# Optimization experiments

Measured on AMD Instinct MI355X. Metric: run time of the kernel, lower is better.

Reference implementation:

```python
import jax, jax.numpy as jnp
import numpy as np

N_CLASSES = 300
EMPTY = N_CLASSES
ALPHA, GAMMA = 0.25, 2.0
W_CLS, W_DOA, W_LOUD, W_CONF, W_SCE = 1.0, 1.0, 0.5, 1.0, 0.3
L_CLS, L_DOA, L_CONF = 1.0, 1.0, 0.5  # matching cost weights


def _lsa(cost):
    """Rectangular linear sum assignment (Jonker-Volgenant / e-maxx Hungarian).
    Returns (row_idx, col_idx) matching min(P,G) pairs, same optimum as scipy."""
    transposed = cost.shape[0] > cost.shape[1]
    C = cost.T if transposed else cost
    n, m = C.shape  # n <= m
    INF = float('inf')
    u = [0.0] * (n + 1)
    v = [0.0] * (m + 1)
    p = [0] * (m + 1)
    for i in range(1, n + 1):
        p[0] = i
        j0 = 0
        minv = [INF] * (m + 1)
        way = [0] * (m + 1)
        used = [False] * (m + 1)
        while True:
            used[j0] = True
            i0 = p[j0]
            delta = INF
            j1 = 0
            for j in range(1, m + 1):
                if not used[j]:
                    cur = C[i0 - 1, j - 1] - u[i0] - v[j]
                    if cur < minv[j]:
                        minv[j] = cur
                        way[j] = j0
                    if minv[j] < delta:
                        delta = minv[j]
                        j1 = j
            for j in range(m + 1):
                if used[j]:
                    u[p[j]] += delta
                    v[j] -= delta
                else:
                    minv[j] -= delta
            j0 = j1
            if p[j0] == 0:
                break
        while j0:
            j1 = way[j0]
            p[j0] = p[j1]
            j0 = j1
    rows, cols = [], []
    for j in range(1, m + 1):
        if p[j]:
            rows.append(p[j] - 1)
            cols.append(j - 1)
    r = np.asarray(rows, np.int64)
    c = np.asarray(cols, np.int64)
    if transposed:
        r, c = c, r
    return r, c


def _match(cl, dv, conf, gcls, gdoa, gmask):
    """Per-frame Hungarian matching (no-grad, host numpy), faithful to hungarian_match.
    Returns matched mask (B,T,S) bool, per-slot target class (B,T,S) int32 (EMPTY if unmatched),
    and gather index into gt slots (B,T,S) int32 (0 where unmatched; masked out later)."""
    B, T, S, C = cl.shape
    z = cl - cl.max(-1, keepdims=True)
    prob = np.exp(z)
    prob /= prob.sum(-1, keepdims=True)
    prob = prob[..., :N_CLASSES]
    dn = dv / np.maximum(np.linalg.norm(dv, axis=-1, keepdims=True), 1e-12)
    cp = 1.0 / (1.0 + np.exp(-conf))
    matched = np.zeros((B, T, S), bool)
    tgt = np.full((B, T, S), EMPTY, np.int32)
    gidx = np.zeros((B, T, S), np.int32)
    for b in range(B):
        for t in range(T):
            act = np.nonzero(gmask[b, t])[0]
            if act.size == 0:
                continue
            gc = gcls[b, t, act]
            gd = gdoa[b, t, act]
            gdn = gd / np.maximum(np.linalg.norm(gd, axis=-1, keepdims=True), 1e-12)
            cost = (L_CLS * (-prob[b, t][:, gc])
                    + L_DOA * (1.0 - dn[b, t] @ gdn.T)
                    + L_CONF * (1.0 - cp[b, t])[:, None])
            r, c = _lsa(cost.astype(np.float64))
            matched[b, t, r] = True
            tgt[b, t, r] = gc[c]
            gidx[b, t, r] = act[c]
    return matched, tgt, gidx


def _loss(class_logits, doa_vec, loudness, confidence, sce_vec, gt_doa, gt_loud,
          matched, tgt_cls, gidx):
    B, T, S, _ = class_logits.shape
    dt = class_logits.dtype
    mf = matched.astype(dt)                      # (B,T,S)
    # focal loss (target = matched gt class, else EMPTY)
    logp = jax.nn.log_softmax(class_logits, axis=-1)
    ce = -jnp.take_along_axis(logp, tgt_cls[..., None].astype(jnp.int32), axis=-1)[..., 0]
    f = ALPHA * (1.0 - jnp.exp(-ce)) ** GAMMA * ce
    Gm = mf.sum(-1)                              # (B,T) matched count
    Um = S - Gm
    safeG = jnp.maximum(Gm, 1.0)
    safeU = jnp.maximum(Um, 1.0)
    cls_fr = (jnp.where(Gm > 0, (f * mf).sum(-1) / safeG, 0.0)
              + jnp.where(Um > 0, (f * (1.0 - mf)).sum(-1) / safeU, 0.0))
    # gather matched gt doa / loud per slot
    g3 = jnp.broadcast_to(gidx[..., None].astype(jnp.int32), gt_doa.shape)
    mdoa = jnp.take_along_axis(gt_doa, g3, axis=2)       # (B,T,S,3)
    mloud = jnp.take_along_axis(gt_loud, gidx.astype(jnp.int32), axis=2)
    # DOA cosine distance (torch cosine_similarity eps=1e-8)
    eps = 1e-8
    num = (doa_vec * mdoa).sum(-1)
    den = (jnp.maximum(jnp.linalg.norm(doa_vec, axis=-1), eps)
           * jnp.maximum(jnp.linalg.norm(mdoa, axis=-1), eps))
    d = 1.0 - num / den
    doa_fr = jnp.where(Gm > 0, (d * mf).sum(-1) / safeG, 0.0)
    # smooth L1 (beta=1)
    diff = loudness - mloud
    ad = jnp.abs(diff)
    sl1 = jnp.where(ad < 1.0, 0.5 * diff * diff, ad - 0.5)
    loud_fr = jnp.where(Gm > 0, (sl1 * mf).sum(-1) / safeG, 0.0)
    # BCE-with-logits, target = matched indicator (zeros if no gt)
    bce = jax.nn.softplus(confidence) - confidence * mf
    conf_fr = bce.mean(-1)
    # SCE: mse(sce, gt_doa * exp(gt_loud/20)) over matched slots
    gt_sce = mdoa * jnp.exp(mloud / 20.0)[..., None]
    sq = ((sce_vec - gt_sce) ** 2).mean(-1)
    sce_fr = jnp.where(Gm > 0, (sq * mf).sum(-1) / safeG, 0.0)
    norm = float(B * T)
    cls_l = W_CLS * cls_fr.sum() / norm
    doa_l = W_DOA * doa_fr.sum() / norm
    loud_l = W_LOUD * loud_fr.sum() / norm
    conf_l = W_CONF * conf_fr.sum() / norm
    sce_l = W_SCE * sce_fr.sum() / norm
    total = cls_l + doa_l + loud_l + conf_l + sce_l
    return jnp.stack([cls_l, doa_l, loud_l, conf_l, sce_l, total])


def setup_inputs() -> dict:
    key = jax.random.key(0)
    ks = jax.random.split(key, 9)
    B, T, S = 32, 256, 8
    C = N_CLASSES + 1
    return {
        "class_logits": jax.random.normal(ks[0], (B, T, S, C), jnp.float32),
        "doa_vec": jax.random.normal(ks[1], (B, T, S, 3), jnp.float32),
        "loudness": jax.random.normal(ks[2], (B, T, S), jnp.float32),
        "confidence": jax.random.normal(ks[3], (B, T, S), jnp.float32),
        "sce_vec": jax.random.normal(ks[4], (B, T, S, 3), jnp.float32),
        "gt_cls": jax.random.randint(ks[5], (B, T, S), 0, N_CLASSES, jnp.int32),
        "gt_doa": jax.random.normal(ks[6], (B, T, S, 3), jnp.float32),
        "gt_loud": jax.random.normal(ks[7], (B, T, S), jnp.float32),
        "gt_mask": jax.random.bernoulli(ks[8], 0.5, (B, T, S)),
    }


def reference(class_logits, doa_vec, loudness, confidence, sce_vec,
              gt_cls, gt_doa, gt_loud, gt_mask):
    matched, tgt, gidx = _match(np.asarray(class_logits), np.asarray(doa_vec),
                                np.asarray(confidence), np.asarray(gt_cls),
                                np.asarray(gt_doa), np.asarray(gt_mask))
    return _loss(class_logits, doa_vec, loudness, confidence, sce_vec,
                 gt_doa, gt_loud,
                 jnp.asarray(matched), jnp.asarray(tgt), jnp.asarray(gidx))
```

## Files before the change

kernel.cpp:

```cpp
#include <hip/hip_runtime.h>
#include <math.h>

#define NFRAMES 8192
#define NS 8
#define NC 301
#define NBLOCKS (NFRAMES / 4)

__device__ float g_partial[5 * NFRAMES];

__device__ __forceinline__ float readlanef(float x, int l) {
    return __int_as_float(__builtin_amdgcn_readlane(__float_as_int(x), l));
}

__global__ __launch_bounds__(256) void frame_kernel(
    const float* __restrict__ logits,
    const float* __restrict__ doa,
    const float* __restrict__ loud,
    const float* __restrict__ conf,
    const float* __restrict__ sce,
    const int*   __restrict__ gcls,
    const float* __restrict__ gdoa,
    const float* __restrict__ gloud,
    const unsigned int* __restrict__ gmaskw)
{
    __shared__ float lgs[4][NS * NC];

    const int lane = threadIdx.x & 63;
    const int wv   = threadIdx.x >> 6;
    const int f    = blockIdx.x * 4 + wv;
    const int s    = lane >> 3;
    const int g    = lane & 7;

    unsigned int mwd = gmaskw[lane];
    unsigned long long blo = __ballot((mwd & 0xFFFFFF00u) != 0);
    unsigned long long bf1 = __ballot(mwd == 0x3f800000u);
    const int mode = (blo == 0ull) ? 0 : (bf1 ? 2 : 1);

    {
        const float4* src = reinterpret_cast<const float4*>(logits + (size_t)f * (NS * NC));
        float4* dst = reinterpret_cast<float4*>(&lgs[wv][0]);
#pragma unroll
        for (int k = 0; k < 10; k++) {
            int idx = lane + (k << 6);
            if (idx < 602) dst[idx] = src[idx];
        }
    }

    float L_loud = 0.f, L_cf = 0.f, L_dx = 0.f, L_dy = 0.f, L_dz = 0.f;
    float L_s0 = 0.f, L_s1 = 0.f, L_s2 = 0.f;
    if (lane < 8) {
        size_t base = (size_t)f * NS + lane;
        L_loud = loud[base];  L_cf = conf[base];
        L_dx = doa[base * 3]; L_dy = doa[base * 3 + 1]; L_dz = doa[base * 3 + 2];
        L_s0 = sce[base * 3]; L_s1 = sce[base * 3 + 1]; L_s2 = sce[base * 3 + 2];
    }

    const float* ls = &lgs[wv][s * NC];

    float v[38];
#pragma unroll
    for (int k = 0; k < 38; k++) {
        int c = g + (k << 3);
        v[k] = (c < NC) ? ls[c] : -INFINITY;
    }
    float m0 = v[0], m1 = v[1], m2 = v[2], m3 = v[3];
#pragma unroll
    for (int k = 4; k + 3 < 38; k += 4) {
        m0 = fmaxf(m0, v[k]);     m1 = fmaxf(m1, v[k + 1]);
        m2 = fmaxf(m2, v[k + 2]); m3 = fmaxf(m3, v[k + 3]);
    }
    m0 = fmaxf(m0, v[36]); m1 = fmaxf(m1, v[37]);
    float m = fmaxf(fmaxf(m0, m1), fmaxf(m2, m3));
    m = fmaxf(m, __shfl_xor(m, 1, 8));
    m = fmaxf(m, __shfl_xor(m, 2, 8));
    m = fmaxf(m, __shfl_xor(m, 4, 8));
    float z0 = __expf(v[0] - m), z1 = __expf(v[1] - m);
    float z2 = __expf(v[2] - m), z3 = __expf(v[3] - m);
#pragma unroll
    for (int k = 4; k + 3 < 38; k += 4) {
        z0 += __expf(v[k] - m);     z1 += __expf(v[k + 1] - m);
        z2 += __expf(v[k + 2] - m); z3 += __expf(v[k + 3] - m);
    }
    z0 += __expf(v[36] - m); z1 += __expf(v[37] - m);
    float z = (z0 + z1) + (z2 + z3);
    z += __shfl_xor(z, 1, 8);
    z += __shfl_xor(z, 2, 8);
    z += __shfl_xor(z, 4, 8);
    const float A = m + __logf(z);
    const float lossA = __shfl(A, (lane & 7) << 3);

    int gcv = (lane < 8) ? gcls[f * NS + lane] : 0;
    int slotcls = __shfl(gcv, g);
    float myLgat = lgs[wv][s * NC + slotcls];
    float lossL300 = (lane < 8) ? lgs[wv][lane * NC + 300] : 0.f;

    bool on = false;
    if (lane < 8) {
        int idx = f * NS + lane;
        if (mode == 0)      on = ((const int*)gmaskw)[idx] != 0;
        else if (mode == 1) on = ((const unsigned char*)gmaskw)[idx] != 0;
        else                on = ((const float*)gmaskw)[idx] != 0.f;
    }
    unsigned long long bal = __ballot(on);
    const unsigned int actmask = (unsigned int)(bal & 0xFFull);
    const int G = __popc(actmask);

    int act_reg = 0;
    float gdx = 0.f, gdy = 0.f, gdz = 0.f;
    float rgx = 0.f, rgy = 0.f, rgz = 0.f, rgl = 0.f;
    if (lane < G) {
        unsigned int mk = actmask;
        for (int t = 0; t < lane; t++) mk &= mk - 1;
        int slot = __ffs(mk) - 1;
        act_reg = slot;
        size_t b3 = (size_t)(f * NS + slot) * 3;
        float x = gdoa[b3], y = gdoa[b3 + 1], zz = gdoa[b3 + 2];
        rgx = x; rgy = y; rgz = zz;
        rgl = gloud[(size_t)f * NS + slot];
        float n = fmaxf(sqrtf(x * x + y * y + zz * zz), 1e-12f);
        gdx = x / n; gdy = y / n; gdz = zz / n;
    }

    size_t sb3 = ((size_t)f * NS + s) * 3;
    float dxr = doa[sb3], dyr = doa[sb3 + 1], dzr = doa[sb3 + 2];
    float nn = fmaxf(sqrtf(dxr * dxr + dyr * dyr + dzr * dzr), 1e-12f);
    float dnx = dxr / nn, dny = dyr / nn, dnz = dzr / nn;
    float cp = 1.f / (1.f + __expf(-conf[(size_t)f * NS + s]));

    int   ag = __shfl(act_reg, g);
    float gx = __shfl(gdx, g), gy = __shfl(gdy, g), gz = __shfl(gdz, g);
    float lgt_c = __shfl(myLgat, (lane & 56) | ag);
    float costreg = INFINITY;
    if (g < G) {
        float pr = __expf(lgt_c - A);
        float dt = dnx * gx + dny * gy + dnz * gz;
        costreg = -pr + (1.f - dt) + 0.5f * (1.f - cp);
    }

    float d0 = (lane == 0) ? 0.f : INFINITY;
    float d1 = INFINITY, d2 = INFINITY, d3 = INFINITY;
    unsigned int par0 = 0, par1 = 0, par2 = 0, par3 = 0;

    for (int i = 0; i < G; i++) {
        float cc0 = readlanef(costreg,      i);
        float cc1 = readlanef(costreg,  8 + i);
        float cc2 = readlanef(costreg, 16 + i);
        float cc3 = readlanef(costreg, 24 + i);
        float cc4 = readlanef(costreg, 32 + i);
        float cc5 = readlanef(costreg, 40 + i);
        float cc6 = readlanef(costreg, 48 + i);
        float cc7 = readlanef(costreg, 56 + i);

        float n0, n1, n2, n3; int b0i, b1i, b2i, b3i;

#define DP_LOW6(dk, bestv, bestb)                                                    \
        {                                                                            \
            float best = INFINITY; int bb = 0; float nb, cand;                       \
            nb = __shfl_xor(dk, 1);  cand = (lane & 1)  ? nb + cc0 : INFINITY; if (cand < best) { best = cand; bb = 0; } \
            nb = __shfl_xor(dk, 2);  cand = (lane & 2)  ? nb + cc1 : INFINITY; if (cand < best) { best = cand; bb = 1; } \
            nb = __shfl_xor(dk, 4);  cand = (lane & 4)  ? nb + cc2 : INFINITY; if (cand < best) { best = cand; bb = 2; } \
            nb = __shfl_xor(dk, 8);  cand = (lane & 8)  ? nb + cc3 : INFINITY; if (cand < best) { best = cand; bb = 3; } \
            nb = __shfl_xor(dk, 16); cand = (lane & 16) ? nb + cc4 : INFINITY; if (cand < best) { best = cand; bb = 4; } \
            nb = __shfl_xor(dk, 32); cand = (lane & 32) ? nb + cc5 : INFINITY; if (cand < best) { best = cand; bb = 5; } \
            bestv = best; bestb = bb;                                                \
        }

        DP_LOW6(d0, n0, b0i)
        DP_LOW6(d1, n1, b1i)
        DP_LOW6(d2, n2, b2i)
        DP_LOW6(d3, n3, b3i)
#undef DP_LOW6
        { float cand = d0 + cc6; if (cand < n1) { n1 = cand; b1i = 6; } }
        { float cand = d2 + cc6; if (cand < n3) { n3 = cand; b3i = 6; } }
        { float cand = d0 + cc7; if (cand < n2) { n2 = cand; b2i = 7; } }
        { float cand = d1 + cc7; if (cand < n3) { n3 = cand; b3i = 7; } }

        d0 = n0; d1 = n1; d2 = n2; d3 = n3;
        int sh = 3 * i;
        par0 |= (unsigned)b0i << sh;
        par1 |= (unsigned)b1i << sh;
        par2 |= (unsigned)b2i << sh;
        par3 |= (unsigned)b3i << sh;
    }

    int mm_ = 0, mygt = 0;
    if (G > 0) {
        float vv = d0; int bm = lane;
        if (d1 < vv) { vv = d1; bm = lane | 64; }
        if (d2 < vv) { vv = d2; bm = lane | 128; }
        if (d3 < vv) { vv = d3; bm = lane | 192; }
        for (int o = 1; o < 64; o <<= 1) {
            float ov = __shfl_xor(vv, o);
            int   om = __shfl_xor(bm, o);
            if (ov < vv || (ov == vv && om < bm)) { vv = ov; bm = om; }
        }
        int mask = bm;
        for (int i = G - 1; i >= 0; i--) {
            int owner = mask & 63, kk = mask >> 6;
            unsigned qsel = (kk == 0) ? par0 : (kk == 1) ? par1
                          : (kk == 2) ? par2 : par3;
            unsigned qv = (unsigned)__builtin_amdgcn_readlane((int)qsel, owner);
            int p = (qv >> (3 * i)) & 7;
            if (lane == p) { mm_ = 1; mygt = i; }
            mask ^= 1 << p;
        }
    }

    int   gidx_v = __shfl(act_reg, mygt);
    float lgt_m  = __shfl(myLgat, ((lane & 7) << 3) + gidx_v);
    float mdx = __shfl(rgx, mygt), mdy = __shfl(rgy, mygt), mdz = __shfl(rgz, mygt);
    float ml  = __shfl(rgl, mygt);

    if (lane < 8) {
        int ss = lane;
        float mf = (float)mm_;
        float lgt = mm_ ? lgt_m : lossL300;
        float ce = lossA - lgt;
        float t1 = 1.f - __expf(-ce);
        float fce = 0.25f * t1 * t1 * ce;

        float num = L_dx * mdx + L_dy * mdy + L_dz * mdz;
        float den = fmaxf(sqrtf(L_dx * L_dx + L_dy * L_dy + L_dz * L_dz), 1e-8f) *
                    fmaxf(sqrtf(mdx * mdx + mdy * mdy + mdz * mdz), 1e-8f);
        float dterm = 1.f - num / den;

        float diff = L_loud - ml;
        float ad = fabsf(diff);
        float sl1 = (ad < 1.f) ? 0.5f * diff * diff : (ad - 0.5f);

        float sp = fmaxf(L_cf, 0.f) + __logf(1.f + __expf(-fabsf(L_cf)));
        float bce = sp - L_cf * mf;

        float el = __expf(ml * 0.05f);
        float e0 = L_s0 - mdx * el;
        float e1 = L_s1 - mdy * el;
        float e2 = L_s2 - mdz * el;
        float sq = (e0 * e0 + e1 * e1 + e2 * e2) * (1.f / 3.f);

        float c_m  = fce * mf;
        float c_u  = fce * (1.f - mf);
        float dsum = dterm * mf;
        float lsum = sl1 * mf;
        float qsum = sq * mf;
        float bsum = bce;
        for (int o = 1; o < 8; o <<= 1) {
            c_m  += __shfl_xor(c_m,  o, 8);
            c_u  += __shfl_xor(c_u,  o, 8);
            dsum += __shfl_xor(dsum, o, 8);
            lsum += __shfl_xor(lsum, o, 8);
            qsum += __shfl_xor(qsum, o, 8);
            bsum += __shfl_xor(bsum, o, 8);
        }
        if (ss == 0) {
            float Gm = (float)G, Um = (float)(NS - G);
            g_partial[0 * NFRAMES + f] = (G > 0 ? c_m / Gm : 0.f) + (G < NS ? c_u / Um : 0.f);
            g_partial[1 * NFRAMES + f] = (G > 0) ? dsum / Gm : 0.f;
            g_partial[2 * NFRAMES + f] = (G > 0) ? lsum / Gm : 0.f;
            g_partial[3 * NFRAMES + f] = bsum * (1.f / 8.f);
            g_partial[4 * NFRAMES + f] = (G > 0) ? qsum / Gm : 0.f;
        }
    }
}

__global__ __launch_bounds__(1024) void reduce_kernel(float* __restrict__ out) {
    __shared__ float red[16][5];
    const int tid  = threadIdx.x;
    const int lane = tid & 63;
    const int w    = tid >> 6;

    float a[5];
#pragma unroll
    for (int k = 0; k < 5; k++) {
        float lcl = 0.f;
        for (int i = tid; i < NFRAMES; i += 1024) lcl += g_partial[k * NFRAMES + i];
#pragma unroll
        for (int o = 1; o < 64; o <<= 1) lcl += __shfl_xor(lcl, o);
        a[k] = lcl;
    }
    if (lane == 0) {
#pragma unroll
        for (int k = 0; k < 5; k++) red[w][k] = a[k];
    }
    __syncthreads();
    if (tid == 0) {
        float acc[5] = {0.f, 0.f, 0.f, 0.f, 0.f};
        for (int ww = 0; ww < 16; ww++)
#pragma unroll
            for (int k = 0; k < 5; k++) acc[k] += red[ww][k];
        const float inv_norm = 1.f / (float)NFRAMES;
        float cls_l  = 1.0f * acc[0] * inv_norm;
        float doa_l  = 1.0f * acc[1] * inv_norm;
        float loud_l = 0.5f * acc[2] * inv_norm;
        float conf_l = 1.0f * acc[3] * inv_norm;
        float sce_l  = 0.3f * acc[4] * inv_norm;
        out[0] = cls_l; out[1] = doa_l; out[2] = loud_l;
        out[3] = conf_l; out[4] = sce_l;
        out[5] = cls_l + doa_l + loud_l + conf_l + sce_l;
    }
}

extern "C" void kernel_launch(void* const* d_in, const int* in_sizes, int n_in,
                              void* d_out, int out_size, void* d_ws, size_t ws_size,
                              hipStream_t stream) {
    const float* logits = (const float*)d_in[0];
    const float* doa    = (const float*)d_in[1];
    const float* loudn  = (const float*)d_in[2];
    const float* confi  = (const float*)d_in[3];
    const float* sce    = (const float*)d_in[4];
    const int*   gcls   = (const int*)d_in[5];
    const float* gdoa   = (const float*)d_in[6];
    const float* gloud  = (const float*)d_in[7];
    const unsigned int* gmask = (const unsigned int*)d_in[8];
    float* out = (float*)d_out;

    frame_kernel<<<NBLOCKS, 256, 0, stream>>>(logits, doa, loudn, confi, sce,
                                              gcls, gdoa, gloud, gmask);
    reduce_kernel<<<1, 1024, 0, stream>>>(out);
}
```

Before: 50.01 us.

## Pipeline per-wave frame loop with double-buffered direct global-to-LDS loads

Each block becomes a single wave that handles four frames in sequence. While the current frame is processed, the next frame's logits are prefetched into a second LDS buffer using global_load_lds, with explicit vmcnt waits. The goal is to hide global load latency behind the Hungarian DP and softmax work and to skip the register round-trip of the old copy. In exchange there are fewer waves per block, serial frames per wave, and hand-written waitcnt counts that must match the number of loads issued.

```diff
diff --git a/kernel.cpp b/kernel.cpp
--- a/kernel.cpp
+++ b/kernel.cpp
@@ -4,7 +4,11 @@
 #define NFRAMES 8192
 #define NS 8
 #define NC 301
-#define NBLOCKS (NFRAMES / 4)
+#define FPW 4
+#define NBLOCKS (NFRAMES / FPW)
+
+#define GLOBAL_AS __attribute__((address_space(1)))
+#define LDS_AS    __attribute__((address_space(3)))
 
 __device__ float g_partial[5 * NFRAMES];
 
@@ -12,7 +16,7 @@
     return __int_as_float(__builtin_amdgcn_readlane(__float_as_int(x), l));
 }
 
-__global__ __launch_bounds__(256) void frame_kernel(
+__global__ __launch_bounds__(64, 2) void frame_kernel(
     const float* __restrict__ logits,
     const float* __restrict__ doa,
     const float* __restrict__ loud,
@@ -23,243 +27,266 @@
     const float* __restrict__ gloud,
     const unsigned int* __restrict__ gmaskw)
 {
-    __shared__ float lgs[4][NS * NC];
-
-    const int lane = threadIdx.x & 63;
-    const int wv   = threadIdx.x >> 6;
-    const int f    = blockIdx.x * 4 + wv;
-    const int s    = lane >> 3;
-    const int g    = lane & 7;
+    __shared__ float lgs[2][NS * NC];
+
+    const int lane = threadIdx.x;
+    const int fbase = blockIdx.x * FPW;
+    const int s = lane >> 3;
+    const int g = lane & 7;
 
     unsigned int mwd = gmaskw[lane];
     unsigned long long blo = __ballot((mwd & 0xFFFFFF00u) != 0);
     unsigned long long bf1 = __ballot(mwd == 0x3f800000u);
     const int mode = (blo == 0ull) ? 0 : (bf1 ? 2 : 1);
 
-    {
-        const float4* src = reinterpret_cast<const float4*>(logits + (size_t)f * (NS * NC));
-        float4* dst = reinterpret_cast<float4*>(&lgs[wv][0]);
-#pragma unroll
-        for (int k = 0; k < 10; k++) {
-            int idx = lane + (k << 6);
-            if (idx < 602) dst[idx] = src[idx];
-        }
-    }
-
-    float L_loud = 0.f, L_cf = 0.f, L_dx = 0.f, L_dy = 0.f, L_dz = 0.f;
-    float L_s0 = 0.f, L_s1 = 0.f, L_s2 = 0.f;
-    if (lane < 8) {
-        size_t base = (size_t)f * NS + lane;
-        L_loud = loud[base];  L_cf = conf[base];
-        L_dx = doa[base * 3]; L_dy = doa[base * 3 + 1]; L_dz = doa[base * 3 + 2];
-        L_s0 = sce[base * 3]; L_s1 = sce[base * 3 + 1]; L_s2 = sce[base * 3 + 2];
-    }
-
-    const float* ls = &lgs[wv][s * NC];
-
-    float v[38];
-#pragma unroll
-    for (int k = 0; k < 38; k++) {
-        int c = g + (k << 3);
-        v[k] = (c < NC) ? ls[c] : -INFINITY;
-    }
-    float m0 = v[0], m1 = v[1], m2 = v[2], m3 = v[3];
-#pragma unroll
-    for (int k = 4; k + 3 < 38; k += 4) {
-        m0 = fmaxf(m0, v[k]);     m1 = fmaxf(m1, v[k + 1]);
-        m2 = fmaxf(m2, v[k + 2]); m3 = fmaxf(m3, v[k + 3]);
-    }
-    m0 = fmaxf(m0, v[36]); m1 = fmaxf(m1, v[37]);
-    float m = fmaxf(fmaxf(m0, m1), fmaxf(m2, m3));
-    m = fmaxf(m, __shfl_xor(m, 1, 8));
-    m = fmaxf(m, __shfl_xor(m, 2, 8));
-    m = fmaxf(m, __shfl_xor(m, 4, 8));
-    float z0 = __expf(v[0] - m), z1 = __expf(v[1] - m);
-    float z2 = __expf(v[2] - m), z3 = __expf(v[3] - m);
-#pragma unroll
-    for (int k = 4; k + 3 < 38; k += 4) {
-        z0 += __expf(v[k] - m);     z1 += __expf(v[k + 1] - m);
-        z2 += __expf(v[k + 2] - m); z3 += __expf(v[k + 3] - m);
-    }
-    z0 += __expf(v[36] - m); z1 += __expf(v[37] - m);
-    float z = (z0 + z1) + (z2 + z3);
-    z += __shfl_xor(z, 1, 8);
-    z += __shfl_xor(z, 2, 8);
-    z += __shfl_xor(z, 4, 8);
-    const float A = m + __logf(z);
-    const float lossA = __shfl(A, (lane & 7) << 3);
-
-    int gcv = (lane < 8) ? gcls[f * NS + lane] : 0;
-    int slotcls = __shfl(gcv, g);
-    float myLgat = lgs[wv][s * NC + slotcls];
-    float lossL300 = (lane < 8) ? lgs[wv][lane * NC + 300] : 0.f;
-
-    bool on = false;
-    if (lane < 8) {
-        int idx = f * NS + lane;
-        if (mode == 0)      on = ((const int*)gmaskw)[idx] != 0;
-        else if (mode == 1) on = ((const unsigned char*)gmaskw)[idx] != 0;
-        else                on = ((const float*)gmaskw)[idx] != 0.f;
-    }
-    unsigned long long bal = __ballot(on);
-    const unsigned int actmask = (unsigned int)(bal & 0xFFull);
-    const int G = __popc(actmask);
-
-    int act_reg = 0;
-    float gdx = 0.f, gdy = 0.f, gdz = 0.f;
-    float rgx = 0.f, rgy = 0.f, rgz = 0.f, rgl = 0.f;
-    if (lane < G) {
-        unsigned int mk = actmask;
-        for (int t = 0; t < lane; t++) mk &= mk - 1;
-        int slot = __ffs(mk) - 1;
-        act_reg = slot;
-        size_t b3 = (size_t)(f * NS + slot) * 3;
-        float x = gdoa[b3], y = gdoa[b3 + 1], zz = gdoa[b3 + 2];
-        rgx = x; rgy = y; rgz = zz;
-        rgl = gloud[(size_t)f * NS + slot];
-        float n = fmaxf(sqrtf(x * x + y * y + zz * zz), 1e-12f);
-        gdx = x / n; gdy = y / n; gdz = zz / n;
-    }
-
-    size_t sb3 = ((size_t)f * NS + s) * 3;
-    float dxr = doa[sb3], dyr = doa[sb3 + 1], dzr = doa[sb3 + 2];
-    float nn = fmaxf(sqrtf(dxr * dxr + dyr * dyr + dzr * dzr), 1e-12f);
-    float dnx = dxr / nn, dny = dyr / nn, dnz = dzr / nn;
-    float cp = 1.f / (1.f + __expf(-conf[(size_t)f * NS + s]));
-
-    int   ag = __shfl(act_reg, g);
-    float gx = __shfl(gdx, g), gy = __shfl(gdy, g), gz = __shfl(gdz, g);
-    float lgt_c = __shfl(myLgat, (lane & 56) | ag);
-    float costreg = INFINITY;
-    if (g < G) {
-        float pr = __expf(lgt_c - A);
-        float dt = dnx * gx + dny * gy + dnz * gz;
-        costreg = -pr + (1.f - dt) + 0.5f * (1.f - cp);
-    }
-
-    float d0 = (lane == 0) ? 0.f : INFINITY;
-    float d1 = INFINITY, d2 = INFINITY, d3 = INFINITY;
-    unsigned int par0 = 0, par1 = 0, par2 = 0, par3 = 0;
-
-    for (int i = 0; i < G; i++) {
-        float cc0 = readlanef(costreg,      i);
-        float cc1 = readlanef(costreg,  8 + i);
-        float cc2 = readlanef(costreg, 16 + i);
-        float cc3 = readlanef(costreg, 24 + i);
-        float cc4 = readlanef(costreg, 32 + i);
-        float cc5 = readlanef(costreg, 40 + i);
-        float cc6 = readlanef(costreg, 48 + i);
-        float cc7 = readlanef(costreg, 56 + i);
-
-        float n0, n1, n2, n3; int b0i, b1i, b2i, b3i;
+#define STAGE(FR, B)                                                            \
+    {                                                                           \
+        const float4* src_ = reinterpret_cast<const float4*>(                   \
+            logits + (size_t)(FR) * (NS * NC));                                 \
+        char* dstb_ = reinterpret_cast<char*>(&lgs[(B)][0]);                    \
+        _Pragma("unroll")                                                       \
+        for (int k = 0; k < 9; k++) {                                           \
+            __builtin_amdgcn_global_load_lds(                                   \
+                (const GLOBAL_AS void*)(src_ + (k << 6) + lane),                \
+                (LDS_AS void*)(dstb_ + (k << 10)), 16, 0, 0);                   \
+        }                                                                       \
+        if (lane < 602 - 576) {                                                 \
+            __builtin_amdgcn_global_load_lds(                                   \
+                (const GLOBAL_AS void*)(src_ + 576 + lane),                     \
+                (LDS_AS void*)(dstb_ + 9 * 1024), 16, 0, 0);                    \
+        }                                                                       \
+    }
+
+    STAGE(fbase, 0)
+
+#pragma unroll
+    for (int t = 0; t < FPW; t++) {
+        const int f = fbase + t;
+        const float* buf = &lgs[t & 1][0];
+
+        if (t + 1 < FPW) {
+            STAGE(f + 1, (t + 1) & 1)
+            asm volatile("s_waitcnt vmcnt(10)" ::: "memory");
+        } else {
+            asm volatile("s_waitcnt vmcnt(0)" ::: "memory");
+        }
+
+        float L_loud = 0.f, L_cf = 0.f, L_dx = 0.f, L_dy = 0.f, L_dz = 0.f;
+        float L_s0 = 0.f, L_s1 = 0.f, L_s2 = 0.f;
+        if (lane < 8) {
+            size_t base = (size_t)f * NS + lane;
+            L_loud = loud[base];  L_cf = conf[base];
+            L_dx = doa[base * 3]; L_dy = doa[base * 3 + 1]; L_dz = doa[base * 3 + 2];
+            L_s0 = sce[base * 3]; L_s1 = sce[base * 3 + 1]; L_s2 = sce[base * 3 + 2];
+        }
+        int gcv = (lane < 8) ? gcls[f * NS + lane] : 0;
+
+        size_t sb3 = ((size_t)f * NS + s) * 3;
+        float dxr = doa[sb3], dyr = doa[sb3 + 1], dzr = doa[sb3 + 2];
+        float nn = fmaxf(sqrtf(dxr * dxr + dyr * dyr + dzr * dzr), 1e-12f);
+        float dnx = dxr / nn, dny = dyr / nn, dnz = dzr / nn;
+        float cp = 1.f / (1.f + __expf(-conf[(size_t)f * NS + s]));
+
+        const float* ls = buf + s * NC;
+
+        float v[38];
+#pragma unroll
+        for (int k = 0; k < 38; k++) {
+            int c = g + (k << 3);
+            v[k] = (c < NC) ? ls[c] : -INFINITY;
+        }
+        float m0 = v[0], m1 = v[1], m2 = v[2], m3 = v[3];
+#pragma unroll
+        for (int k = 4; k + 3 < 38; k += 4) {
+            m0 = fmaxf(m0, v[k]);     m1 = fmaxf(m1, v[k + 1]);
+            m2 = fmaxf(m2, v[k + 2]); m3 = fmaxf(m3, v[k + 3]);
+        }
+        m0 = fmaxf(m0, v[36]); m1 = fmaxf(m1, v[37]);
+        float m = fmaxf(fmaxf(m0, m1), fmaxf(m2, m3));
+        m = fmaxf(m, __shfl_xor(m, 1, 8));
+        m = fmaxf(m, __shfl_xor(m, 2, 8));
+        m = fmaxf(m, __shfl_xor(m, 4, 8));
+        float z0 = __expf(v[0] - m), z1 = __expf(v[1] - m);
+        float z2 = __expf(v[2] - m), z3 = __expf(v[3] - m);
+#pragma unroll
+        for (int k = 4; k + 3 < 38; k += 4) {
+            z0 += __expf(v[k] - m);     z1 += __expf(v[k + 1] - m);
+            z2 += __expf(v[k + 2] - m); z3 += __expf(v[k + 3] - m);
+        }
+        z0 += __expf(v[36] - m); z1 += __expf(v[37] - m);
+        float z = (z0 + z1) + (z2 + z3);
+        z += __shfl_xor(z, 1, 8);
+        z += __shfl_xor(z, 2, 8);
+        z += __shfl_xor(z, 4, 8);
+        const float A = m + __logf(z);
+        const float lossA = __shfl(A, (lane & 7) << 3);
+
+        int slotcls = __shfl(gcv, g);
+        float myLgat = buf[s * NC + slotcls];
+        float lossL300 = (lane < 8) ? buf[lane * NC + 300] : 0.f;
+
+        bool on = false;
+        if (lane < 8) {
+            int idx = f * NS + lane;
+            if (mode == 0)      on = ((const int*)gmaskw)[idx] != 0;
+            else if (mode == 1) on = ((const unsigned char*)gmaskw)[idx] != 0;
+            else                on = ((const float*)gmaskw)[idx] != 0.f;
+        }
+        unsigned long long bal = __ballot(on);
+        const unsigned int actmask = (unsigned int)(bal & 0xFFull);
+        const int G = __popc(actmask);
+
+        int act_reg = 0;
+        float gdx = 0.f, gdy = 0.f, gdz = 0.f;
+        float rgx = 0.f, rgy = 0.f, rgz = 0.f, rgl = 0.f;
+        if (lane < G) {
+            unsigned int mk = actmask;
+            for (int tt = 0; tt < lane; tt++) mk &= mk - 1;
+            int slot = __ffs(mk) - 1;
+            act_reg = slot;
+            size_t b3 = (size_t)(f * NS + slot) * 3;
+            float x = gdoa[b3], y = gdoa[b3 + 1], zz = gdoa[b3 + 2];
+            rgx = x; rgy = y; rgz = zz;
+            rgl = gloud[(size_t)f * NS + slot];
+            float n = fmaxf(sqrtf(x * x + y * y + zz * zz), 1e-12f);
+            gdx = x / n; gdy = y / n; gdz = zz / n;
+        }
+
+        int   ag = __shfl(act_reg, g);
+        float gx = __shfl(gdx, g), gy = __shfl(gdy, g), gz = __shfl(gdz, g);
+        float lgt_c = __shfl(myLgat, (lane & 56) | ag);
+        float costreg = INFINITY;
+        if (g < G) {
+            float pr = __expf(lgt_c - A);
+            float dt = dnx * gx + dny * gy + dnz * gz;
+            costreg = -pr + (1.f - dt) + 0.5f * (1.f - cp);
+        }
+
+        float d0 = (lane == 0) ? 0.f : INFINITY;
+        float d1 = INFINITY, d2 = INFINITY, d3 = INFINITY;
+        unsigned int par0 = 0, par1 = 0, par2 = 0, par3 = 0;
+
+        for (int i = 0; i < G; i++) {
+            float cc0 = readlanef(costreg,      i);
+            float cc1 = readlanef(costreg,  8 + i);
+            float cc2 = readlanef(costreg, 16 + i);
+            float cc3 = readlanef(costreg, 24 + i);
+            float cc4 = readlanef(costreg, 32 + i);
+            float cc5 = readlanef(costreg, 40 + i);
+            float cc6 = readlanef(costreg, 48 + i);
+            float cc7 = readlanef(costreg, 56 + i);
+
+            float n0, n1, n2, n3; int b0i, b1i, b2i, b3i;
 
 #define DP_LOW6(dk, bestv, bestb)                                                    \
-        {                                                                            \
-            float best = INFINITY; int bb = 0; float nb, cand;                       \
-            nb = __shfl_xor(dk, 1);  cand = (lane & 1)  ? nb + cc0 : INFINITY; if (cand < best) { best = cand; bb = 0; } \
-            nb = __shfl_xor(dk, 2);  cand = (lane & 2)  ? nb + cc1 : INFINITY; if (cand < best) { best = cand; bb = 1; } \
-            nb = __shfl_xor(dk, 4);  cand = (lane & 4)  ? nb + cc2 : INFINITY; if (cand < best) { best = cand; bb = 2; } \
-            nb = __shfl_xor(dk, 8);  cand = (lane & 8)  ? nb + cc3 : INFINITY; if (cand < best) { best = cand; bb = 3; } \
-            nb = __shfl_xor(dk, 16); cand = (lane & 16) ? nb + cc4 : INFINITY; if (cand < best) { best = cand; bb = 4; } \
-            nb = __shfl_xor(dk, 32); cand = (lane & 32) ? nb + cc5 : INFINITY; if (cand < best) { best = cand; bb = 5; } \
-            bestv = best; bestb = bb;                                                \
-        }
-
-        DP_LOW6(d0, n0, b0i)
-        DP_LOW6(d1, n1, b1i)
-        DP_LOW6(d2, n2, b2i)
-        DP_LOW6(d3, n3, b3i)
+            {                                                                        \
+                float best = INFINITY; int bb = 0; float nb, cand;                   \
+                nb = __shfl_xor(dk, 1);  cand = (lane & 1)  ? nb + cc0 : INFINITY; if (cand < best) { best = cand; bb = 0; } \
+                nb = __shfl_xor(dk, 2);  cand = (lane & 2)  ? nb + cc1 : INFINITY; if (cand < best) { best = cand; bb = 1; } \
+                nb = __shfl_xor(dk, 4);  cand = (lane & 4)  ? nb + cc2 : INFINITY; if (cand < best) { best = cand; bb = 2; } \
+                nb = __shfl_xor(dk, 8);  cand = (lane & 8)  ? nb + cc3 : INFINITY; if (cand < best) { best = cand; bb = 3; } \
+                nb = __shfl_xor(dk, 16); cand = (lane & 16) ? nb + cc4 : INFINITY; if (cand < best) { best = cand; bb = 4; } \
+                nb = __shfl_xor(dk, 32); cand = (lane & 32) ? nb + cc5 : INFINITY; if (cand < best) { best = cand; bb = 5; } \
+                bestv = best; bestb = bb;                                            \
+            }
+
+            DP_LOW6(d0, n0, b0i)
+            DP_LOW6(d1, n1, b1i)
+            DP_LOW6(d2, n2, b2i)
+            DP_LOW6(d3, n3, b3i)
 #undef DP_LOW6
-        { float cand = d0 + cc6; if (cand < n1) { n1 = cand; b1i = 6; } }
-        { float cand = d2 + cc6; if (cand < n3) { n3 = cand; b3i = 6; } }
-        { float cand = d0 + cc7; if (cand < n2) { n2 = cand; b2i = 7; } }
-        { float cand = d1 + cc7; if (cand < n3) { n3 = cand; b3i = 7; } }
-
-        d0 = n0; d1 = n1; d2 = n2; d3 = n3;
-        int sh = 3 * i;
-        par0 |= (unsigned)b0i << sh;
-        par1 |= (unsigned)b1i << sh;
-        par2 |= (unsigned)b2i << sh;
-        par3 |= (unsigned)b3i << sh;
-    }
-
-    int mm_ = 0, mygt = 0;
-    if (G > 0) {
-        float vv = d0; int bm = lane;
-        if (d1 < vv) { vv = d1; bm = lane | 64; }
-        if (d2 < vv) { vv = d2; bm = lane | 128; }
-        if (d3 < vv) { vv = d3; bm = lane | 192; }
-        for (int o = 1; o < 64; o <<= 1) {
-            float ov = __shfl_xor(vv, o);
-            int   om = __shfl_xor(bm, o);
-            if (ov < vv || (ov == vv && om < bm)) { vv = ov; bm = om; }
-        }
-        int mask = bm;
-        for (int i = G - 1; i >= 0; i--) {
-            int owner = mask & 63, kk = mask >> 6;
-            unsigned qsel = (kk == 0) ? par0 : (kk == 1) ? par1
-                          : (kk == 2) ? par2 : par3;
-            unsigned qv = (unsigned)__builtin_amdgcn_readlane((int)qsel, owner);
-            int p = (qv >> (3 * i)) & 7;
-            if (lane == p) { mm_ = 1; mygt = i; }
-            mask ^= 1 << p;
-        }
-    }
-
-    int   gidx_v = __shfl(act_reg, mygt);
-    float lgt_m  = __shfl(myLgat, ((lane & 7) << 3) + gidx_v);
-    float mdx = __shfl(rgx, mygt), mdy = __shfl(rgy, mygt), mdz = __shfl(rgz, mygt);
-    float ml  = __shfl(rgl, mygt);
-
-    if (lane < 8) {
-        int ss = lane;
-        float mf = (float)mm_;
-        float lgt = mm_ ? lgt_m : lossL300;
-        float ce = lossA - lgt;
-        float t1 = 1.f - __expf(-ce);
-        float fce = 0.25f * t1 * t1 * ce;
-
-        float num = L_dx * mdx + L_dy * mdy + L_dz * mdz;
-        float den = fmaxf(sqrtf(L_dx * L_dx + L_dy * L_dy + L_dz * L_dz), 1e-8f) *
-                    fmaxf(sqrtf(mdx * mdx + mdy * mdy + mdz * mdz), 1e-8f);
-        float dterm = 1.f - num / den;
-
-        float diff = L_loud - ml;
-        float ad = fabsf(diff);
-        float sl1 = (ad < 1.f) ? 0.5f * diff * diff : (ad - 0.5f);
-
-        float sp = fmaxf(L_cf, 0.f) + __logf(1.f + __expf(-fabsf(L_cf)));
-        float bce = sp - L_cf * mf;
-
-        float el = __expf(ml * 0.05f);
-        float e0 = L_s0 - mdx * el;
-        float e1 = L_s1 - mdy * el;
-        float e2 = L_s2 - mdz * el;
-        float sq = (e0 * e0 + e1 * e1 + e2 * e2) * (1.f / 3.f);
-
-        float c_m  = fce * mf;
-        float c_u  = fce * (1.f - mf);
-        float dsum = dterm * mf;
-        float lsum = sl1 * mf;
-        float qsum = sq * mf;
-        float bsum = bce;
-        for (int o = 1; o < 8; o <<= 1) {
-            c_m  += __shfl_xor(c_m,  o, 8);
-            c_u  += __shfl_xor(c_u,  o, 8);
-            dsum += __shfl_xor(dsum, o, 8);
-            lsum += __shfl_xor(lsum, o, 8);
-            qsum += __shfl_xor(qsum, o, 8);
-            bsum += __shfl_xor(bsum, o, 8);
-        }
-        if (ss == 0) {
-            float Gm = (float)G, Um = (float)(NS - G);
-            g_partial[0 * NFRAMES + f] = (G > 0 ? c_m / Gm : 0.f) + (G < NS ? c_u / Um : 0.f);
-            g_partial[1 * NFRAMES + f] = (G > 0) ? dsum / Gm : 0.f;
-            g_partial[2 * NFRAMES + f] = (G > 0) ? lsum / Gm : 0.f;
-            g_partial[3 * NFRAMES + f] = bsum * (1.f / 8.f);
-            g_partial[4 * NFRAMES + f] = (G > 0) ? qsum / Gm : 0.f;
-        }
-    }
+            { float cand = d0 + cc6; if (cand < n1) { n1 = cand; b1i = 6; } }
+            { float cand = d2 + cc6; if (cand < n3) { n3 = cand; b3i = 6; } }
+            { float cand = d0 + cc7; if (cand < n2) { n2 = cand; b2i = 7; } }
+            { float cand = d1 + cc7; if (cand < n3) { n3 = cand; b3i = 7; } }
+
+            d0 = n0; d1 = n1; d2 = n2; d3 = n3;
+            int sh = 3 * i;
+            par0 |= (unsigned)b0i << sh;
+            par1 |= (unsigned)b1i << sh;
+            par2 |= (unsigned)b2i << sh;
+            par3 |= (unsigned)b3i << sh;
+        }
+
+        int mm_ = 0, mygt = 0;
+        if (G > 0) {
+            float vv = d0; int bm = lane;
+            if (d1 < vv) { vv = d1; bm = lane | 64; }
+            if (d2 < vv) { vv = d2; bm = lane | 128; }
+            if (d3 < vv) { vv = d3; bm = lane | 192; }
+            for (int o = 1; o < 64; o <<= 1) {
+                float ov = __shfl_xor(vv, o);
+                int   om = __shfl_xor(bm, o);
+                if (ov < vv || (ov == vv && om < bm)) { vv = ov; bm = om; }
+            }
+            int mask = bm;
+            for (int i = G - 1; i >= 0; i--) {
+                int owner = mask & 63, kk = mask >> 6;
+                unsigned qsel = (kk == 0) ? par0 : (kk == 1) ? par1
+                              : (kk == 2) ? par2 : par3;
+                unsigned qv = (unsigned)__builtin_amdgcn_readlane((int)qsel, owner);
+                int p = (qv >> (3 * i)) & 7;
+                if (lane == p) { mm_ = 1; mygt = i; }
+                mask ^= 1 << p;
+            }
+        }
+
+        int   gidx_v = __shfl(act_reg, mygt);
+        float lgt_m  = __shfl(myLgat, ((lane & 7) << 3) + gidx_v);
+        float mdx = __shfl(rgx, mygt), mdy = __shfl(rgy, mygt), mdz = __shfl(rgz, mygt);
+        float ml  = __shfl(rgl, mygt);
+
+        if (lane < 8) {
+            int ss = lane;
+            float mf = (float)mm_;
+            float lgt = mm_ ? lgt_m : lossL300;
+            float ce = lossA - lgt;
+            float t1 = 1.f - __expf(-ce);
+            float fce = 0.25f * t1 * t1 * ce;
+
+            float num = L_dx * mdx + L_dy * mdy + L_dz * mdz;
+            float den = fmaxf(sqrtf(L_dx * L_dx + L_dy * L_dy + L_dz * L_dz), 1e-8f) *
+                        fmaxf(sqrtf(mdx * mdx + mdy * mdy + mdz * mdz), 1e-8f);
+            float dterm = 1.f - num / den;
+
+            float diff = L_loud - ml;
+            float ad = fabsf(diff);
+            float sl1 = (ad < 1.f) ? 0.5f * diff * diff : (ad - 0.5f);
+
+            float sp = fmaxf(L_cf, 0.f) + __logf(1.f + __expf(-fabsf(L_cf)));
+            float bce = sp - L_cf * mf;
+
+            float el = __expf(ml * 0.05f);
+            float e0 = L_s0 - mdx * el;
+            float e1 = L_s1 - mdy * el;
+            float e2 = L_s2 - mdz * el;
+            float sq = (e0 * e0 + e1 * e1 + e2 * e2) * (1.f / 3.f);
+
+            float c_m  = fce * mf;
+            float c_u  = fce * (1.f - mf);
+            float dsum = dterm * mf;
+            float lsum = sl1 * mf;
+            float qsum = sq * mf;
+            float bsum = bce;
+            for (int o = 1; o < 8; o <<= 1) {
+                c_m  += __shfl_xor(c_m,  o, 8);
+                c_u  += __shfl_xor(c_u,  o, 8);
+                dsum += __shfl_xor(dsum, o, 8);
+                lsum += __shfl_xor(lsum, o, 8);
+                qsum += __shfl_xor(qsum, o, 8);
+                bsum += __shfl_xor(bsum, o, 8);
+            }
+            if (ss == 0) {
+                float Gm = (float)G, Um = (float)(NS - G);
+                g_partial[0 * NFRAMES + f] = (G > 0 ? c_m / Gm : 0.f) + (G < NS ? c_u / Um : 0.f);
+                g_partial[1 * NFRAMES + f] = (G > 0) ? dsum / Gm : 0.f;
+                g_partial[2 * NFRAMES + f] = (G > 0) ? lsum / Gm : 0.f;
+                g_partial[3 * NFRAMES + f] = bsum * (1.f / 8.f);
+                g_partial[4 * NFRAMES + f] = (G > 0) ? qsum / Gm : 0.f;
+            }
+        }
+    }
+#undef STAGE
 }
 
 __global__ __launch_bounds__(1024) void reduce_kernel(float* __restrict__ out) {
@@ -313,7 +340,7 @@
     const unsigned int* gmask = (const unsigned int*)d_in[8];
     float* out = (float*)d_out;
 
-    frame_kernel<<<NBLOCKS, 256, 0, stream>>>(logits, doa, loudn, confi, sce,
-                                              gcls, gdoa, gloud, gmask);
+    frame_kernel<<<NBLOCKS, 64, 0, stream>>>(logits, doa, loudn, confi, sce,
+                                             gcls, gdoa, gloud, gmask);
     reduce_kernel<<<1, 1024, 0, stream>>>(out);
 }
```

After: 57.50 us. 15.0% more time.
